# Kernel tuning notes

Hardware: AMD Instinct MI355X
Metric: run time of the kernel (lower is better)

The kernel has to match this reference:

```python
import jax, jax.numpy as jnp
import numpy as np

NEG_INF = -1e9
LRELU_SLOPE = 0.2  # torch GAT default leaky_relu negative slope


def setup_inputs() -> dict:
    key = jax.random.key(0)
    k1, k2, k3, k4, k5 = jax.random.split(key, 5)
    N, F_IN, H, DH = 4096, 1433, 8, 8  # n_nodes, in_features, n_heads, per-head dim (n_hidden=64)
    vert = jax.random.normal(k1, (N, F_IN), dtype=jnp.float32)
    edge = jax.random.randint(k2, (N, N), 0, 2, dtype=jnp.int32)  # dense adjacency mask
    W = jax.random.normal(k3, (F_IN, H * DH), dtype=jnp.float32) * 0.05
    a_l = jax.random.normal(k4, (H, DH), dtype=jnp.float32) * 0.05
    a_r = jax.random.normal(k5, (H, DH), dtype=jnp.float32) * 0.05
    return {"vert": vert, "edge": edge, "W": W, "a_l": a_l, "a_r": a_r}


def reference(vert, edge, W, a_l, a_r):
    # GAT-style edge-affinity layer (is_concat=True) + ELU; dropout is identity (eval mode).
    N = vert.shape[0]
    H, DH = a_l.shape
    g = (vert @ W).reshape(N, H, DH)                      # [N,H,Dh] projected node features
    sl = jnp.einsum('nhd,hd->nh', g, a_l)                 # source-node attention term
    sr = jnp.einsum('nhd,hd->nh', g, a_r)                 # target-node attention term
    e = sl[:, None, :] + sr[None, :, :]                   # [N,N,H]: attn([g_i || g_j])
    e = jnp.where(e >= 0, e, LRELU_SLOPE * e)             # leaky_relu
    mask = (edge != 0)[:, :, None]                        # [N,N,1]
    e = jnp.where(mask, e, NEG_INF)                       # mask non-edges
    a = jax.nn.softmax(e, axis=1)                         # normalize over neighbors j
    out = jnp.einsum('ijh,jhd->ihd', a, g).reshape(N, H * DH)  # aggregate + concat heads
    return jax.nn.elu(out)
```

## Files before the change

kernel.cpp:

```cpp
#include <hip/hip_runtime.h>
#include <hip/hip_bf16.h>

#define NN 4096
#define FIN 1433
#define NH 8
#define DH 8
#define HD 64
#define KP 1472
#define LOG2E 1.44269504f
#define NJS 8
#define NCHK ((NN / NJS) / 128)
#define NKS 4

typedef unsigned int u32;
typedef unsigned long long u64;
typedef float v4f __attribute__((ext_vector_type(4)));
typedef _Float16 f16;
typedef _Float16 h2 __attribute__((ext_vector_type(2)));
typedef _Float16 f16x8 __attribute__((ext_vector_type(8)));

static __device__ __forceinline__ short f2h16(float f) {
    union { f16 h; short s; } u; u.h = (f16)f; return u.s;
}
static __device__ __forceinline__ h2 u2h2(u32 x) {
    union { u32 u; h2 h; } v; v.u = x; return v.h;
}
static __device__ __forceinline__ u32 h22u(h2 x) {
    union { h2 h; u32 u; } v; v.h = x; return v.u;
}

#if __has_builtin(__builtin_amdgcn_sbfe)
#define SBFE1(x, k) __builtin_amdgcn_sbfe((int)(x), (k), 1)
#else
#define SBFE1(x, k) (((int)((x) << (31 - (k)))) >> 31)
#endif

static __device__ __forceinline__ void gload_lds16(const void* g, void* l) {
    __builtin_amdgcn_global_load_lds(
        (const __attribute__((address_space(1))) void*)g,
        (__attribute__((address_space(3))) void*)l, 16, 0, 0);
}

__global__ __launch_bounds__(256) void k_eprep(const int* __restrict__ edge,
                                               uint4* __restrict__ emask) {
    const int t = threadIdx.x, lane = t & 63, w = t >> 6;
    const int row = blockIdx.x;
    const int* erow = edge + (size_t)row * NN;
    uint4* mrow = emask + (size_t)row * (NN / 128);
#pragma unroll
    for (int it = 0; it < 8; ++it) {
        const int ck = w * 8 + it;
        const int2 e2 = *(const int2*)&erow[ck * 128 + 2 * lane];
        const u64 bA = __ballot(e2.x != 0);
        const u64 bB = __ballot(e2.y != 0);
        if (lane == 0)
            mrow[ck] = (uint4){(u32)bA, (u32)(bA >> 32), (u32)bB, (u32)(bB >> 32)};
    }
}

__global__ __launch_bounds__(256) void k_wprep(const float* __restrict__ W,
                                               short* __restrict__ Wt) {
    __shared__ float Ts[64][65];
    const int c = blockIdx.x;
    const int u = threadIdx.x;
    const int n4 = (u & 15) * 4;
    const int kr = u >> 4;
#pragma unroll
    for (int q = 0; q < 4; ++q) {
        const int kl = kr + q * 16;
        const int kg = c * 64 + kl;
        v4f v = {0.f, 0.f, 0.f, 0.f};
        if (kg < FIN) v = *(const v4f*)&W[(size_t)kg * HD + n4];
        *(v4f*)&Ts[kl][n4] = v;
    }
    __syncthreads();
    const int n = u >> 2;
    const int koff = (u & 3) * 16;
    __align__(16) short tmp[16];
#pragma unroll
    for (int r = 0; r < 16; ++r) tmp[r] = f2h16(Ts[koff + r][n]);
    *(uint4*)&Wt[(size_t)n * KP + c * 64 + koff]     = *(uint4*)&tmp[0];
    *(uint4*)&Wt[(size_t)n * KP + c * 64 + koff + 8] = *(uint4*)&tmp[8];
}

__global__ __launch_bounds__(256, 4) void k_gemm(
    const float* __restrict__ vert, const short* __restrict__ Wt,
    float* __restrict__ Cp)
{
    __shared__ float cacc[4][16][68];

    const int t = threadIdx.x, lane = t & 63, w = t >> 6;
    const int ml = lane & 15, q = lane >> 4;
    const int i0 = blockIdx.x * 16;
    const int ks = blockIdx.y;
    const float* vrow = vert + (size_t)(i0 + ml) * FIN;

    v4f acc[4];
#pragma unroll
    for (int g = 0; g < 4; ++g) acc[g] = (v4f){0.f, 0.f, 0.f, 0.f};

    for (int c = ks + 4 * w; c < 45; c += 16) {
        const int k0 = c * 32 + q * 8;
        v4f a0, a1;
        if (k0 + 7 < FIN) {
            a0 = *(const v4f*)&vrow[k0];
            a1 = *(const v4f*)&vrow[k0 + 4];
        } else {
            float tmp[8];
#pragma unroll
            for (int e = 0; e < 8; ++e)
                tmp[e] = (k0 + e < FIN) ? vrow[k0 + e] : 0.f;
            a0 = (v4f){tmp[0], tmp[1], tmp[2], tmp[3]};
            a1 = (v4f){tmp[4], tmp[5], tmp[6], tmp[7]};
        }
        const f16x8 af = {(f16)a0.x, (f16)a0.y, (f16)a0.z, (f16)a0.w,
                          (f16)a1.x, (f16)a1.y, (f16)a1.z, (f16)a1.w};
#pragma unroll
        for (int g = 0; g < 4; ++g) {
            const f16x8 bf = *(const f16x8*)&Wt[(size_t)(g * 16 + ml) * KP + k0];
            acc[g] = __builtin_amdgcn_mfma_f32_16x16x32_f16(af, bf, acc[g], 0, 0, 0);
        }
    }

#pragma unroll
    for (int g = 0; g < 4; ++g)
#pragma unroll
        for (int r = 0; r < 4; ++r)
            cacc[w][q * 4 + r][g * 16 + ml] = acc[g][r];
    __syncthreads();

    const int m = t >> 4, n4 = (t & 15) * 4;
    v4f s = (v4f){0.f, 0.f, 0.f, 0.f};
#pragma unroll
    for (int ww = 0; ww < 4; ++ww) s += *(const v4f*)&cacc[ww][m][n4];
    *(v4f*)&Cp[((size_t)ks * NN + i0 + m) * HD + n4] = s;
}

__global__ __launch_bounds__(256) void k_gpost(
    const float* __restrict__ Cp,
    const float* __restrict__ al, const float* __restrict__ ar,
    short* __restrict__ gT, short* __restrict__ eB, short* __restrict__ eD,
    float* __restrict__ Rw)
{
    const int t = threadIdx.x;
    const int gid = blockIdx.x * 256 + t;
    const int i = gid >> 4, n4 = (gid & 15) * 4;

    v4f s = (v4f){0.f, 0.f, 0.f, 0.f};
#pragma unroll
    for (int ks = 0; ks < NKS; ++ks)
        s += *(const v4f*)&Cp[((size_t)ks * NN + i) * HD + n4];

#pragma unroll
    for (int e = 0; e < 4; ++e)
        gT[(size_t)(n4 + e) * NN + i] = f2h16(s[e]);

    float pl = s.x * al[n4] + s.y * al[n4 + 1] + s.z * al[n4 + 2] + s.w * al[n4 + 3];
    float pr = s.x * ar[n4] + s.y * ar[n4 + 1] + s.z * ar[n4 + 2] + s.w * ar[n4 + 3];
    pl += __shfl_xor(pl, 1, 64);
    pr += __shfl_xor(pr, 1, 64);
    if ((t & 1) == 0) {
        const int h = (t & 15) >> 1;
        eB[h * NN + i] = f2h16(exp2f(pr * LOG2E));
        eD[h * NN + i] = f2h16(exp2f(0.2f * pr * LOG2E));
        Rw[i * NH + h] = exp2f(-0.8f * pl * LOG2E);
    }
}

__global__ __launch_bounds__(256, 8) void k_attn(
    const uint4* __restrict__ emask, const short* __restrict__ gT,
    const short* __restrict__ eB, const short* __restrict__ eD,
    const float* __restrict__ Rw,
    float* __restrict__ numw, float* __restrict__ denw)
{
    __shared__ __align__(16) short Gs[64 * 128];
    __shared__ __align__(16) short BDs[8 * 256];

    const int t = threadIdx.x, lane = t & 63, w = t >> 6;
    const int ml = lane & 15, quad = lane >> 4;
    const int m8 = ml & 7;
    const int i0 = blockIdx.x * 16;
    const int js = blockIdx.y;
    const int jbase = js * (NN / NJS);
    const int h0 = w, h1 = w + 4;
    const int qb4 = quad * 4;
    const bool mhi = (ml >= 8);
    const u32 one2 = 0x3C003C00u;
    const uint4 ones4 = (uint4){one2, one2, one2, one2};

    h2 Ri[2];
    {
        const f16 r0 = (f16)Rw[(i0 + ml) * NH + h0];
        const f16 r1 = (f16)Rw[(i0 + ml) * NH + h1];
        Ri[0] = (h2){r0, r0};
        Ri[1] = (h2){r1, r1};
    }

    const uint4* mrow = emask + (size_t)(i0 + ml) * (NN / 128) + js * NCHK;

    const short* gsrc[4];
#pragma unroll
    for (int r = 0; r < 4; ++r) {
        const int u = r * 256 + t;
        const int row = u >> 4;
        const int col = ((u & 15) * 8) ^ ((row & 7) * 8);
        gsrc[r] = gT + (size_t)row * NN + jbase + col;
    }
    const int bh2 = t >> 5, bk = t & 31;
    const short* bdsrc = (bk < 16 ? eB : eD) + (size_t)bh2 * NN + jbase + (bk & 15) * 8;
    char* const gdst = (char*)Gs + (t & ~63) * 16;
    char* const bddst = (char*)BDs + (t & ~63) * 16;

    v4f acc[2];
    acc[0] = (v4f){0.f, 0.f, 0.f, 0.f};
    acc[1] = (v4f){0.f, 0.f, 0.f, 0.f};

    for (int c = 0; c < NCHK; ++c) {
        const int jc = c * 128;
#pragma unroll
        for (int r = 0; r < 4; ++r)
            gload_lds16(gsrc[r] + jc, (char*)Gs + r * 4096 + (t & ~63) * 16);
        gload_lds16(bdsrc + jc, bddst);
        const uint4 mw = mrow[c];
        __syncthreads();
#pragma unroll
        for (int s = 0; s < 4; ++s) {
            const int xj = s * 32 + quad * 8;
            const int xg = xj ^ (m8 * 8);
            const uint4 gu0 = *(const uint4*)&Gs[(h0 * 8 + m8) * 128 + xg];
            const uint4 gu1 = *(const uint4*)&Gs[(h1 * 8 + m8) * 128 + xg];
            const uint4 bu0 = *(const uint4*)&BDs[h0 * 256 + xj];
            const uint4 du0 = *(const uint4*)&BDs[h0 * 256 + 128 + xj];
            const uint4 bu1 = *(const uint4*)&BDs[h1 * 256 + xj];
            const uint4 du1 = *(const uint4*)&BDs[h1 * 256 + 128 + xj];
            const int base = ((s & 1) << 4) + qb4;
            const u32 WA = ((s >> 1) ? mw.y : mw.x) >> base;
            const u32 WB = ((s >> 1) ? mw.w : mw.z) >> base;
            u32 m[4];
#pragma unroll
            for (int k = 0; k < 4; ++k) {
                const int ea = SBFE1(WA, k);
                const int eb = SBFE1(WB, k);
                m[k] = __builtin_amdgcn_perm((u32)eb, (u32)ea, 0x05040100u);
            }
            u32 aw0[4], aw1[4];
#pragma unroll
            for (int k = 0; k < 4; ++k) {
                const u32 rd0 = h22u(Ri[0] * u2h2((&du0.x)[k]));
                const u32 rd1 = h22u(Ri[1] * u2h2((&du1.x)[k]));
                u32 p0, p1;
                asm("v_pk_max_f16 %0, %1, %2" : "=v"(p0) : "v"(rd0), "v"((&bu0.x)[k]));
                asm("v_pk_max_f16 %0, %1, %2" : "=v"(p1) : "v"(rd1), "v"((&bu1.x)[k]));
                aw0[k] = p0 & m[k];
                aw1[k] = p1 & m[k];
            }
            union { uint4 u; f16x8 h; } a0u, a1u, g0u, g1u;
            a0u.u = (uint4){aw0[0], aw0[1], aw0[2], aw0[3]};
            a1u.u = (uint4){aw1[0], aw1[1], aw1[2], aw1[3]};
            g0u.u = mhi ? ones4 : gu0;
            g1u.u = mhi ? ones4 : gu1;
            acc[0] = __builtin_amdgcn_mfma_f32_16x16x32_f16(a0u.h, g0u.h, acc[0], 0, 0, 0);
            acc[1] = __builtin_amdgcn_mfma_f32_16x16x32_f16(a1u.h, g1u.h, acc[1], 0, 0, 0);
        }
        __syncthreads();
    }

    float* nw = numw + (size_t)js * NN * HD;
    float* dw = denw + (size_t)js * NN * NH;
    const int ibase = i0 + quad * 4;
#pragma unroll
    for (int hh = 0; hh < 2; ++hh) {
        const int h = w + hh * 4;
#pragma unroll
        for (int r = 0; r < 4; ++r) {
            if (ml < 8)       nw[(ibase + r) * HD + h * 8 + ml] = acc[hh][r];
            else if (ml == 8) dw[(ibase + r) * NH + h]          = acc[hh][r];
        }
    }
}

__global__ __launch_bounds__(256) void k_comb(
    const float* __restrict__ numw, const float* __restrict__ denw,
    float* __restrict__ out)
{
    const int gid = blockIdx.x * 256 + threadIdx.x;
    const int i = gid >> 6, h = (gid & 63) >> 3;
    float num = 0.f, den = 0.f;
#pragma unroll
    for (int s = 0; s < NJS; ++s) {
        num += numw[s * NN * HD + gid];
        den += denw[s * NN * NH + i * NH + h];
    }
    float x = num / den;
    out[gid] = (x > 0.f) ? x : (__expf(x) - 1.f);
}

extern "C" void kernel_launch(void* const* d_in, const int* in_sizes, int n_in,
                              void* d_out, int out_size, void* d_ws, size_t ws_size,
                              hipStream_t stream) {
    const float* vert = (const float*)d_in[0];
    const int*   edge = (const int*)d_in[1];
    const float* W    = (const float*)d_in[2];
    const float* al   = (const float*)d_in[3];
    const float* ar   = (const float*)d_in[4];
    float* out = (float*)d_out;

    char* ws = (char*)d_ws;
    short* gT    = (short*)ws;
    short* eB    = (short*)(ws + 512 * 1024);
    short* eD    = (short*)(ws + 576 * 1024);
    float* Rw    = (float*)(ws + 640 * 1024);
    short* Wt    = (short*)(ws + 768 * 1024);
    uint4* emask = (uint4*)(ws + 1024 * 1024);
    float* Cp    = (float*)(ws + 3 * 1024 * 1024);
    float* numw  = (float*)(ws + 7 * 1024 * 1024);
    float* denw  = (float*)(ws + 15 * 1024 * 1024);

    hipLaunchKernelGGL(k_eprep, dim3(NN), dim3(256), 0, stream, edge, emask);
    hipLaunchKernelGGL(k_wprep, dim3(23), dim3(256), 0, stream, W, Wt);
    hipLaunchKernelGGL(k_gemm, dim3(NN / 16, NKS), dim3(256), 0, stream,
                       vert, Wt, Cp);
    hipLaunchKernelGGL(k_gpost, dim3(NN * 16 / 256), dim3(256), 0, stream,
                       Cp, al, ar, gT, eB, eD, Rw);
    hipLaunchKernelGGL(k_attn, dim3(NN / 16, NJS), dim3(256), 0, stream,
                       emask, gT, eB, eD, Rw, numw, denw);
    hipLaunchKernelGGL(k_comb, dim3(NN * HD / 256), dim3(256), 0, stream,
                       numw, denw, out);
}
```

Before: 153.8 us.

## Fuse edge-mask prep, GEMM post-processing and final combine into fewer kernels

Cuts six launches down to three. Edge-mask bit packing moves into the GEMM kernel, and the last split-K block per row tile, chosen with an atomic counter, does the feature post-processing. The combine and ELU step is folded into the attention kernel the same way, using a last-arriving-block counter. This removes launch overhead and inter-kernel gaps, at the cost of extra fences and atomics, and of tail work done by a single wave per tile.

```diff
diff --git a/kernel.cpp b/kernel.cpp
--- a/kernel.cpp
+++ b/kernel.cpp
@@ -41,28 +41,13 @@
         (__attribute__((address_space(3))) void*)l, 16, 0, 0);
 }
 
-__global__ __launch_bounds__(256) void k_eprep(const int* __restrict__ edge,
-                                               uint4* __restrict__ emask) {
-    const int t = threadIdx.x, lane = t & 63, w = t >> 6;
-    const int row = blockIdx.x;
-    const int* erow = edge + (size_t)row * NN;
-    uint4* mrow = emask + (size_t)row * (NN / 128);
-#pragma unroll
-    for (int it = 0; it < 8; ++it) {
-        const int ck = w * 8 + it;
-        const int2 e2 = *(const int2*)&erow[ck * 128 + 2 * lane];
-        const u64 bA = __ballot(e2.x != 0);
-        const u64 bB = __ballot(e2.y != 0);
-        if (lane == 0)
-            mrow[ck] = (uint4){(u32)bA, (u32)(bA >> 32), (u32)bB, (u32)(bB >> 32)};
-    }
-}
-
 __global__ __launch_bounds__(256) void k_wprep(const float* __restrict__ W,
-                                               short* __restrict__ Wt) {
+                                               short* __restrict__ Wt,
+                                               int* __restrict__ cnt) {
     __shared__ float Ts[64][65];
     const int c = blockIdx.x;
     const int u = threadIdx.x;
+    if (c == 0) { cnt[u] = 0; cnt[256 + u] = 0; }
     const int n4 = (u & 15) * 4;
     const int kr = u >> 4;
 #pragma unroll
@@ -83,18 +68,42 @@
     *(uint4*)&Wt[(size_t)n * KP + c * 64 + koff + 8] = *(uint4*)&tmp[8];
 }
 
-__global__ __launch_bounds__(256, 4) void k_gemm(
+__global__ __launch_bounds__(256, 4) void k_mid(
     const float* __restrict__ vert, const short* __restrict__ Wt,
-    float* __restrict__ Cp)
+    const int* __restrict__ edge,
+    const float* __restrict__ al, const float* __restrict__ ar,
+    float* __restrict__ Cp, uint4* __restrict__ emask,
+    short* __restrict__ gT, short* __restrict__ eB, short* __restrict__ eD,
+    float* __restrict__ Rw, int* __restrict__ cntG)
 {
     __shared__ float cacc[4][16][68];
 
     const int t = threadIdx.x, lane = t & 63, w = t >> 6;
     const int ml = lane & 15, q = lane >> 4;
-    const int i0 = blockIdx.x * 16;
+    const int ib = blockIdx.x;
     const int ks = blockIdx.y;
+    const int i0 = ib * 16;
+
+    {
+        const int b = ks * 256 + ib;
+        for (int r = 0; r < 4; ++r) {
+            const int row = b * 4 + r;
+            const int* erow = edge + (size_t)row * NN;
+            uint4* mrow = emask + (size_t)row * (NN / 128);
+#pragma unroll
+            for (int it = 0; it < 8; ++it) {
+                const int ck = w * 8 + it;
+                const int2 e2 = *(const int2*)&erow[ck * 128 + 2 * lane];
+                const u64 bA = __ballot(e2.x != 0);
+                const u64 bB = __ballot(e2.y != 0);
+                if (lane == 0)
+                    mrow[ck] = (uint4){(u32)bA, (u32)(bA >> 32),
+                                       (u32)bB, (u32)(bB >> 32)};
+            }
+        }
+    }
+
     const float* vrow = vert + (size_t)(i0 + ml) * FIN;
-
     v4f acc[4];
 #pragma unroll
     for (int g = 0; g < 4; ++g) acc[g] = (v4f){0.f, 0.f, 0.f, 0.f};
@@ -129,41 +138,47 @@
             cacc[w][q * 4 + r][g * 16 + ml] = acc[g][r];
     __syncthreads();
 
-    const int m = t >> 4, n4 = (t & 15) * 4;
-    v4f s = (v4f){0.f, 0.f, 0.f, 0.f};
-#pragma unroll
-    for (int ww = 0; ww < 4; ++ww) s += *(const v4f*)&cacc[ww][m][n4];
-    *(v4f*)&Cp[((size_t)ks * NN + i0 + m) * HD + n4] = s;
-}
-
-__global__ __launch_bounds__(256) void k_gpost(
-    const float* __restrict__ Cp,
-    const float* __restrict__ al, const float* __restrict__ ar,
-    short* __restrict__ gT, short* __restrict__ eB, short* __restrict__ eD,
-    float* __restrict__ Rw)
-{
-    const int t = threadIdx.x;
-    const int gid = blockIdx.x * 256 + t;
-    const int i = gid >> 4, n4 = (gid & 15) * 4;
-
-    v4f s = (v4f){0.f, 0.f, 0.f, 0.f};
-#pragma unroll
-    for (int ks = 0; ks < NKS; ++ks)
-        s += *(const v4f*)&Cp[((size_t)ks * NN + i) * HD + n4];
-
-#pragma unroll
-    for (int e = 0; e < 4; ++e)
-        gT[(size_t)(n4 + e) * NN + i] = f2h16(s[e]);
-
-    float pl = s.x * al[n4] + s.y * al[n4 + 1] + s.z * al[n4 + 2] + s.w * al[n4 + 3];
-    float pr = s.x * ar[n4] + s.y * ar[n4 + 1] + s.z * ar[n4 + 2] + s.w * ar[n4 + 3];
-    pl += __shfl_xor(pl, 1, 64);
-    pr += __shfl_xor(pr, 1, 64);
-    if ((t & 1) == 0) {
-        const int h = (t & 15) >> 1;
-        eB[h * NN + i] = f2h16(exp2f(pr * LOG2E));
-        eD[h * NN + i] = f2h16(exp2f(0.2f * pr * LOG2E));
-        Rw[i * NH + h] = exp2f(-0.8f * pl * LOG2E);
+    {
+        const int m = t >> 4, n4 = (t & 15) * 4;
+        v4f s = (v4f){0.f, 0.f, 0.f, 0.f};
+#pragma unroll
+        for (int ww = 0; ww < 4; ++ww) s += *(const v4f*)&cacc[ww][m][n4];
+        *(v4f*)&Cp[((size_t)ks * NN + i0 + m) * HD + n4] = s;
+    }
+
+    __threadfence();
+    __syncthreads();
+    int old = 0;
+    if (t == 0) old = atomicAdd(&cntG[ib], 1);
+    if (w == 0) {
+        old = __shfl(old, 0, 64);
+        if (old == NKS - 1) {
+            __threadfence();
+#pragma unroll
+            for (int p = 0; p < 4; ++p) {
+                const int u2 = p * 64 + lane;
+                const int i = i0 + (u2 >> 4), n4 = (u2 & 15) * 4;
+                v4f s = (v4f){0.f, 0.f, 0.f, 0.f};
+#pragma unroll
+                for (int kk = 0; kk < NKS; ++kk)
+                    s += *(const v4f*)&Cp[((size_t)kk * NN + i) * HD + n4];
+#pragma unroll
+                for (int e = 0; e < 4; ++e)
+                    gT[(size_t)(n4 + e) * NN + i] = f2h16(s[e]);
+                float pl = s.x * al[n4] + s.y * al[n4 + 1]
+                         + s.z * al[n4 + 2] + s.w * al[n4 + 3];
+                float pr = s.x * ar[n4] + s.y * ar[n4 + 1]
+                         + s.z * ar[n4 + 2] + s.w * ar[n4 + 3];
+                pl += __shfl_xor(pl, 1, 64);
+                pr += __shfl_xor(pr, 1, 64);
+                if ((u2 & 1) == 0) {
+                    const int h = (u2 & 15) >> 1;
+                    eB[h * NN + i] = f2h16(exp2f(pr * LOG2E));
+                    eD[h * NN + i] = f2h16(exp2f(0.2f * pr * LOG2E));
+                    Rw[i * NH + h] = exp2f(-0.8f * pl * LOG2E);
+                }
+            }
+        }
     }
 }
 
@@ -171,7 +186,8 @@
     const uint4* __restrict__ emask, const short* __restrict__ gT,
     const short* __restrict__ eB, const short* __restrict__ eD,
     const float* __restrict__ Rw,
-    float* __restrict__ numw, float* __restrict__ denw)
+    float* __restrict__ numw, float* __restrict__ denw,
+    float* __restrict__ out, int* __restrict__ cntA)
 {
     __shared__ __align__(16) short Gs[64 * 128];
     __shared__ __align__(16) short BDs[8 * 256];
@@ -179,7 +195,8 @@
     const int t = threadIdx.x, lane = t & 63, w = t >> 6;
     const int ml = lane & 15, quad = lane >> 4;
     const int m8 = ml & 7;
-    const int i0 = blockIdx.x * 16;
+    const int ib = blockIdx.x;
+    const int i0 = ib * 16;
     const int js = blockIdx.y;
     const int jbase = js * (NN / NJS);
     const int h0 = w, h1 = w + 4;
@@ -208,7 +225,6 @@
     }
     const int bh2 = t >> 5, bk = t & 31;
     const short* bdsrc = (bk < 16 ? eB : eD) + (size_t)bh2 * NN + jbase + (bk & 15) * 8;
-    char* const gdst = (char*)Gs + (t & ~63) * 16;
     char* const bddst = (char*)BDs + (t & ~63) * 16;
 
     v4f acc[2];
@@ -277,22 +293,30 @@
             else if (ml == 8) dw[(ibase + r) * NH + h]          = acc[hh][r];
         }
     }
-}
-
-__global__ __launch_bounds__(256) void k_comb(
-    const float* __restrict__ numw, const float* __restrict__ denw,
-    float* __restrict__ out)
-{
-    const int gid = blockIdx.x * 256 + threadIdx.x;
-    const int i = gid >> 6, h = (gid & 63) >> 3;
-    float num = 0.f, den = 0.f;
-#pragma unroll
-    for (int s = 0; s < NJS; ++s) {
-        num += numw[s * NN * HD + gid];
-        den += denw[s * NN * NH + i * NH + h];
-    }
-    float x = num / den;
-    out[gid] = (x > 0.f) ? x : (__expf(x) - 1.f);
+
+    __threadfence();
+    __syncthreads();
+    int old = 0;
+    if (t == 0) old = atomicAdd(&cntA[ib], 1);
+    if (w == 0) {
+        old = __shfl(old, 0, 64);
+        if (old == NJS - 1) {
+            __threadfence();
+#pragma unroll
+            for (int p = 0; p < 16; ++p) {
+                const int row = i0 + p;
+                const int hh = lane >> 3;
+                float num = 0.f, den = 0.f;
+#pragma unroll
+                for (int s = 0; s < NJS; ++s) {
+                    num += numw[(size_t)s * NN * HD + row * HD + lane];
+                    den += denw[(size_t)s * NN * NH + row * NH + hh];
+                }
+                const float x = num / den;
+                out[row * HD + lane] = (x > 0.f) ? x : (__expf(x) - 1.f);
+            }
+        }
+    }
 }
 
 extern "C" void kernel_launch(void* const* d_in, const int* in_sizes, int n_in,
@@ -315,15 +339,11 @@
     float* Cp    = (float*)(ws + 3 * 1024 * 1024);
     float* numw  = (float*)(ws + 7 * 1024 * 1024);
     float* denw  = (float*)(ws + 15 * 1024 * 1024);
-
-    hipLaunchKernelGGL(k_eprep, dim3(NN), dim3(256), 0, stream, edge, emask);
-    hipLaunchKernelGGL(k_wprep, dim3(23), dim3(256), 0, stream, W, Wt);
-    hipLaunchKernelGGL(k_gemm, dim3(NN / 16, NKS), dim3(256), 0, stream,
-                       vert, Wt, Cp);
-    hipLaunchKernelGGL(k_gpost, dim3(NN * 16 / 256), dim3(256), 0, stream,
-                       Cp, al, ar, gT, eB, eD, Rw);
+    int*   cnt   = (int*)(ws + 16 * 1024 * 1024);
+
+    hipLaunchKernelGGL(k_wprep, dim3(23), dim3(256), 0, stream, W, Wt, cnt);
+    hipLaunchKernelGGL(k_mid, dim3(NN / 16, NKS), dim3(256), 0, stream,
+                       vert, Wt, edge, al, ar, Cp, emask, gT, eB, eD, Rw, cnt);
     hipLaunchKernelGGL(k_attn, dim3(NN / 16, NJS), dim3(256), 0, stream,
-                       emask, gT, eB, eD, Rw, numw, denw);
-    hipLaunchKernelGGL(k_comb, dim3(NN * HD / 256), dim3(256), 0, stream,
-                       numw, denw, out);
-}
+                       emask, gT, eB, eD, Rw, numw, denw, out, cnt + 256);
+}
```

After: 558.4 us. 263% more time.

## Fuse edge-mask prep into GEMM kernel and double-buffer attention chunk loads

Applied to the files above, without the earlier changes.

The separate edge-bitmask kernel is folded into the projection GEMM kernel. Each of its 1024 blocks packs four adjacency rows before starting its GEMM slice, which removes one launch and lets the mask pass overlap the GEMM. The attention kernel now works on 64-column chunks with double-buffered LDS staging and a prefetched mask word, so the async global-to-LDS loads for the next chunk overlap the MFMA work on the current one, with one barrier per iteration. The mask word layout is reordered so each 64-column chunk reads a uint2. The cost is more loop iterations, and the GEMM blocks now also carry the heavy 64MB edge read.

```diff
diff --git a/kernel.cpp b/kernel.cpp
--- a/kernel.cpp
+++ b/kernel.cpp
@@ -9,7 +9,7 @@
 #define KP 1472
 #define LOG2E 1.44269504f
 #define NJS 8
-#define NCHK ((NN / NJS) / 128)
+#define NCHK ((NN / NJS) / 64)
 #define NKS 4
 
 typedef unsigned int u32;
@@ -39,23 +39,6 @@
     __builtin_amdgcn_global_load_lds(
         (const __attribute__((address_space(1))) void*)g,
         (__attribute__((address_space(3))) void*)l, 16, 0, 0);
-}
-
-__global__ __launch_bounds__(256) void k_eprep(const int* __restrict__ edge,
-                                               uint4* __restrict__ emask) {
-    const int t = threadIdx.x, lane = t & 63, w = t >> 6;
-    const int row = blockIdx.x;
-    const int* erow = edge + (size_t)row * NN;
-    uint4* mrow = emask + (size_t)row * (NN / 128);
-#pragma unroll
-    for (int it = 0; it < 8; ++it) {
-        const int ck = w * 8 + it;
-        const int2 e2 = *(const int2*)&erow[ck * 128 + 2 * lane];
-        const u64 bA = __ballot(e2.x != 0);
-        const u64 bB = __ballot(e2.y != 0);
-        if (lane == 0)
-            mrow[ck] = (uint4){(u32)bA, (u32)(bA >> 32), (u32)bB, (u32)(bB >> 32)};
-    }
 }
 
 __global__ __launch_bounds__(256) void k_wprep(const float* __restrict__ W,
@@ -83,18 +66,39 @@
     *(uint4*)&Wt[(size_t)n * KP + c * 64 + koff + 8] = *(uint4*)&tmp[8];
 }
 
-__global__ __launch_bounds__(256, 4) void k_gemm(
+__global__ __launch_bounds__(256, 4) void k_mid(
     const float* __restrict__ vert, const short* __restrict__ Wt,
-    float* __restrict__ Cp)
+    const int* __restrict__ edge,
+    float* __restrict__ Cp, uint4* __restrict__ emask)
 {
     __shared__ float cacc[4][16][68];
 
     const int t = threadIdx.x, lane = t & 63, w = t >> 6;
     const int ml = lane & 15, q = lane >> 4;
-    const int i0 = blockIdx.x * 16;
+    const int ib = blockIdx.x;
     const int ks = blockIdx.y;
+    const int i0 = ib * 16;
+
+    {
+        const int b = ks * 256 + ib;
+        for (int r = 0; r < 4; ++r) {
+            const int row = b * 4 + r;
+            const int* erow = edge + (size_t)row * NN;
+            uint4* mrow = emask + (size_t)row * (NN / 128);
+#pragma unroll
+            for (int it = 0; it < 8; ++it) {
+                const int ck = w * 8 + it;
+                const int2 e2 = *(const int2*)&erow[ck * 128 + 2 * lane];
+                const u64 bA = __ballot(e2.x != 0);
+                const u64 bB = __ballot(e2.y != 0);
+                if (lane == 0)
+                    mrow[ck] = (uint4){(u32)bA, (u32)bB,
+                                       (u32)(bA >> 32), (u32)(bB >> 32)};
+            }
+        }
+    }
+
     const float* vrow = vert + (size_t)(i0 + ml) * FIN;
-
     v4f acc[4];
 #pragma unroll
     for (int g = 0; g < 4; ++g) acc[g] = (v4f){0.f, 0.f, 0.f, 0.f};
@@ -173,8 +177,8 @@
     const float* __restrict__ Rw,
     float* __restrict__ numw, float* __restrict__ denw)
 {
-    __shared__ __align__(16) short Gs[64 * 128];
-    __shared__ __align__(16) short BDs[8 * 256];
+    __shared__ __align__(16) short Gs[2][64 * 64];
+    __shared__ __align__(16) short BDs[2][8 * 128];
 
     const int t = threadIdx.x, lane = t & 63, w = t >> 6;
     const int ml = lane & 15, quad = lane >> 4;
@@ -196,46 +200,55 @@
         Ri[1] = (h2){r1, r1};
     }
 
-    const uint4* mrow = emask + (size_t)(i0 + ml) * (NN / 128) + js * NCHK;
-
-    const short* gsrc[4];
-#pragma unroll
-    for (int r = 0; r < 4; ++r) {
-        const int u = r * 256 + t;
-        const int row = u >> 4;
-        const int col = ((u & 15) * 8) ^ ((row & 7) * 8);
-        gsrc[r] = gT + (size_t)row * NN + jbase + col;
-    }
-    const int bh2 = t >> 5, bk = t & 31;
-    const short* bdsrc = (bk < 16 ? eB : eD) + (size_t)bh2 * NN + jbase + (bk & 15) * 8;
-    char* const gdst = (char*)Gs + (t & ~63) * 16;
-    char* const bddst = (char*)BDs + (t & ~63) * 16;
+    const uint2* mrow = (const uint2*)emask + (size_t)(i0 + ml) * (NN / 64) + js * NCHK;
+
+    const short *gsrc0, *gsrc1;
+    {
+        int u = t, row = u >> 3;
+        gsrc0 = gT + (size_t)row * NN + jbase + (((u & 7) * 8) ^ ((row & 7) * 8));
+        u = 256 + t; row = u >> 3;
+        gsrc1 = gT + (size_t)row * NN + jbase + (((u & 7) * 8) ^ ((row & 7) * 8));
+    }
+    const short* bdsrc = nullptr;
+    if (t < 128) {
+        const int head = t >> 4, slot = t & 15;
+        bdsrc = (slot < 8 ? eB : eD) + (size_t)head * NN + jbase + (slot & 7) * 8;
+    }
+    const int wub = (t & ~63) * 16;
+
+#define STAGE(buf, ck)                                                        \
+    do {                                                                      \
+        const int jc_ = (ck) * 64;                                            \
+        gload_lds16(gsrc0 + jc_, (char*)Gs[buf] + wub);                       \
+        gload_lds16(gsrc1 + jc_, (char*)Gs[buf] + 4096 + wub);                \
+        if (t < 128) gload_lds16(bdsrc + jc_, (char*)BDs[buf] + wub);         \
+    } while (0)
 
     v4f acc[2];
     acc[0] = (v4f){0.f, 0.f, 0.f, 0.f};
     acc[1] = (v4f){0.f, 0.f, 0.f, 0.f};
 
+    STAGE(0, 0);
+    uint2 mw = mrow[0], pm;
+
     for (int c = 0; c < NCHK; ++c) {
-        const int jc = c * 128;
-#pragma unroll
-        for (int r = 0; r < 4; ++r)
-            gload_lds16(gsrc[r] + jc, (char*)Gs + r * 4096 + (t & ~63) * 16);
-        gload_lds16(bdsrc + jc, bddst);
-        const uint4 mw = mrow[c];
+        const int cb = c & 1, nb = cb ^ 1;
         __syncthreads();
-#pragma unroll
-        for (int s = 0; s < 4; ++s) {
+        const bool pf = (c + 1) < NCHK;
+        if (pf) { STAGE(nb, c + 1); pm = mrow[c + 1]; }
+#pragma unroll
+        for (int s = 0; s < 2; ++s) {
             const int xj = s * 32 + quad * 8;
             const int xg = xj ^ (m8 * 8);
-            const uint4 gu0 = *(const uint4*)&Gs[(h0 * 8 + m8) * 128 + xg];
-            const uint4 gu1 = *(const uint4*)&Gs[(h1 * 8 + m8) * 128 + xg];
-            const uint4 bu0 = *(const uint4*)&BDs[h0 * 256 + xj];
-            const uint4 du0 = *(const uint4*)&BDs[h0 * 256 + 128 + xj];
-            const uint4 bu1 = *(const uint4*)&BDs[h1 * 256 + xj];
-            const uint4 du1 = *(const uint4*)&BDs[h1 * 256 + 128 + xj];
-            const int base = ((s & 1) << 4) + qb4;
-            const u32 WA = ((s >> 1) ? mw.y : mw.x) >> base;
-            const u32 WB = ((s >> 1) ? mw.w : mw.z) >> base;
+            const uint4 gu0 = *(const uint4*)&Gs[cb][(h0 * 8 + m8) * 64 + xg];
+            const uint4 gu1 = *(const uint4*)&Gs[cb][(h1 * 8 + m8) * 64 + xg];
+            const uint4 bu0 = *(const uint4*)&BDs[cb][h0 * 128 + xj];
+            const uint4 du0 = *(const uint4*)&BDs[cb][h0 * 128 + 64 + xj];
+            const uint4 bu1 = *(const uint4*)&BDs[cb][h1 * 128 + xj];
+            const uint4 du1 = *(const uint4*)&BDs[cb][h1 * 128 + 64 + xj];
+            const int base = (s << 4) + qb4;
+            const u32 WA = mw.x >> base;
+            const u32 WB = mw.y >> base;
             u32 m[4];
 #pragma unroll
             for (int k = 0; k < 4; ++k) {
@@ -262,8 +275,9 @@
             acc[0] = __builtin_amdgcn_mfma_f32_16x16x32_f16(a0u.h, g0u.h, acc[0], 0, 0, 0);
             acc[1] = __builtin_amdgcn_mfma_f32_16x16x32_f16(a1u.h, g1u.h, acc[1], 0, 0, 0);
         }
-        __syncthreads();
-    }
+        if (pf) mw = pm;
+    }
+#undef STAGE
 
     float* nw = numw + (size_t)js * NN * HD;
     float* dw = denw + (size_t)js * NN * NH;
@@ -288,8 +302,8 @@
     float num = 0.f, den = 0.f;
 #pragma unroll
     for (int s = 0; s < NJS; ++s) {
-        num += numw[s * NN * HD + gid];
-        den += denw[s * NN * NH + i * NH + h];
+        num += numw[(size_t)s * NN * HD + gid];
+        den += denw[(size_t)s * NN * NH + i * NH + h];
     }
     float x = num / den;
     out[gid] = (x > 0.f) ? x : (__expf(x) - 1.f);
@@ -316,10 +330,9 @@
     float* numw  = (float*)(ws + 7 * 1024 * 1024);
     float* denw  = (float*)(ws + 15 * 1024 * 1024);
 
-    hipLaunchKernelGGL(k_eprep, dim3(NN), dim3(256), 0, stream, edge, emask);
     hipLaunchKernelGGL(k_wprep, dim3(23), dim3(256), 0, stream, W, Wt);
-    hipLaunchKernelGGL(k_gemm, dim3(NN / 16, NKS), dim3(256), 0, stream,
-                       vert, Wt, Cp);
+    hipLaunchKernelGGL(k_mid, dim3(NN / 16, NKS), dim3(256), 0, stream,
+                       vert, Wt, edge, Cp, emask);
     hipLaunchKernelGGL(k_gpost, dim3(NN * 16 / 256), dim3(256), 0, stream,
                        Cp, al, ar, gT, eB, eD, Rw);
     hipLaunchKernelGGL(k_attn, dim3(NN / 16, NJS), dim3(256), 0, stream,
```

New measurement: 167.0 us. +8.6%, slower.
